# Kernel tuning notes

Measured on AMD Instinct MI355X. Metric: run time of the kernel, lower is better.

Reference implementation:

```python
import jax, jax.numpy as jnp
import numpy as np
from jax import lax

EPS = 1e-10

def _safe_norm(x):
    # torch remove_zeros: replace exact-zero norms with 1e-10
    n = jnp.linalg.norm(x, axis=-1, keepdims=True)
    return jnp.where(n != 0, n, jnp.full_like(n, EPS))

def setup_inputs() -> dict:
    key = jax.random.key(0)
    ks = jax.random.split(key, 5)
    S, B, D = 2048, 32, 512  # seq, batch, 2*hidden
    K = 147  # odd(max_entries/14)
    return {
        "encoder_outputs": jax.random.normal(ks[0], (S, B, D), dtype=jnp.float32),
        "state": jax.random.normal(ks[1], (B, D), dtype=jnp.float32),
        "previous_attention": jax.random.uniform(ks[2], (B, S), dtype=jnp.float32),
        "W_att": jax.random.normal(ks[3], (D, D), dtype=jnp.float32) / np.sqrt(D),
        "b_att": jax.random.normal(ks[4], (D,), dtype=jnp.float32) * 0.01,
        "conv_w": jnp.ones((1, 1, K), dtype=jnp.float32),
        "conv_b": jnp.zeros((1,), dtype=jnp.float32),
    }

def reference(encoder_outputs, state, previous_attention, W_att, b_att, conv_w, conv_b):
    S, B, D = encoder_outputs.shape
    # attended state via linear layer, then cosine-similarity weights (vectorized over seq)
    attended = state @ W_att.T + b_att                       # [B, D]
    ns = attended / _safe_norm(attended)                     # [B, D]
    ne = encoder_outputs / _safe_norm(encoder_outputs)       # [S, B, D]
    weights = jnp.einsum('bd,sbd->bs', ns, ne)               # [B, S]
    # conv1d time smoothing of previous attention (same-length, odd kernel)
    k = conv_w.shape[-1]
    pad = k // 2
    y = lax.conv_general_dilated(previous_attention[:, None, :], conv_w,
                                 window_strides=(1,), padding=[(pad, pad)])
    adjusted = jax.nn.relu(y[:, 0, :] + conv_b)              # [B, S]
    prev_probs = adjusted / jnp.sum(adjusted, axis=1, keepdims=True)
    adj = prev_probs * jax.nn.softmax(weights, axis=1)
    norm_w = adj / jnp.sum(adj, axis=1, keepdims=True)       # [B, S]
    applied = jnp.einsum('bs,sbd->bd', norm_w, encoder_outputs)  # [B, D]
    return applied, norm_w
```

## Files before the change

kernel.cpp:

```cpp
#include <hip/hip_runtime.h>
#include <hip/hip_bf16.h>
#include <math.h>


__device__ __forceinline__ float wave_sum(float v) {
    for (int off = 32; off; off >>= 1) v += __shfl_xor(v, off);
    return v;
}

__global__ __launch_bounds__(256) void front_kernel(
    const float* __restrict__ state, const float* __restrict__ W,
    const float* __restrict__ bias, const float* __restrict__ prev,
    const float* __restrict__ cw, const float* __restrict__ cb,
    float* __restrict__ attended, float* __restrict__ adj,
    int S, int D, int K) {
    __shared__ __align__(16) float smem[1024];
    int b = blockIdx.y;
    int t = threadIdx.x;

    if (blockIdx.x < 2) {
        if (t < D / 4)
            ((float4*)smem)[t] = ((const float4*)(state + (size_t)b * D))[t];
        __syncthreads();
        int d = blockIdx.x * 256 + t;
        const float4* Wrow = (const float4*)(W + (size_t)d * D);
        const float4* sv = (const float4*)smem;
        float acc = bias[d];
#pragma unroll 8
        for (int k = 0; k < 128; ++k) {
            float4 w4 = Wrow[k];
            float4 s4 = sv[k];
            acc += w4.x * s4.x + w4.y * s4.y + w4.z * s4.z + w4.w * s4.w;
        }
        attended[(size_t)b * D + d] = acc;
    } else {
        int s0 = (blockIdx.x - 2) * 256;
        int pad = K / 2;
        int seglen = 256 + K - 1;
        float* seg = smem;
        float* wk = smem + 512;
        for (int i = t; i < seglen; i += 256) {
            int s = s0 - pad + i;
            seg[i] = (s >= 0 && s < S) ? prev[(size_t)b * S + s] : 0.f;
        }
        for (int j = t; j < K; j += 256) wk[j] = cw[j];
        __syncthreads();
        float y = cb[0];
        for (int j = 0; j < K; ++j) y += seg[t + j] * wk[j];
        adj[(size_t)b * S + s0 + t] = fmaxf(y, 0.f);
    }
}

__global__ __launch_bounds__(256) void main_kernel(
    const float* __restrict__ e, const float* __restrict__ attended,
    const float* __restrict__ adj, float* __restrict__ partial,
    float* __restrict__ zbuf, float* __restrict__ u,
    int S, int B, int D, int CH) {
    int wave = threadIdx.x >> 6;
    int lane = threadIdx.x & 63;
    int c = blockIdx.x * 4 + wave;
    int b = blockIdx.y;

    const float4* att4 = (const float4*)(attended + (size_t)b * D);
    float4 a0 = att4[lane];
    float4 a1 = att4[lane + 64];
    float asq = a0.x * a0.x + a0.y * a0.y + a0.z * a0.z + a0.w * a0.w
              + a1.x * a1.x + a1.y * a1.y + a1.z * a1.z + a1.w * a1.w;
    asq = wave_sum(asq);
    float an = sqrtf(asq);
    if (an == 0.f) an = 1e-10f;
    float ainv = 1.f / an;
    float4 ns0, ns1;
    ns0.x = a0.x * ainv; ns0.y = a0.y * ainv; ns0.z = a0.z * ainv; ns0.w = a0.w * ainv;
    ns1.x = a1.x * ainv; ns1.y = a1.y * ainv; ns1.z = a1.z * ainv; ns1.w = a1.w * ainv;

    float4 acc0 = {0.f, 0.f, 0.f, 0.f};
    float4 acc1 = {0.f, 0.f, 0.f, 0.f};
    float z = 0.f;

    int s0 = c * CH;
    const float4* row4 = (const float4*)(e + ((size_t)s0 * B + b) * D);
    size_t rstride = (size_t)B * D / 4;

    float4 x0 = row4[lane];
    float4 x1 = row4[lane + 64];
    for (int i = 0; i < CH; ++i) {
        float4 nx0, nx1;
        if (i + 1 < CH) {
            nx0 = row4[rstride + lane];
            nx1 = row4[rstride + lane + 64];
        }
        float dot = x0.x * ns0.x + x0.y * ns0.y + x0.z * ns0.z + x0.w * ns0.w
                  + x1.x * ns1.x + x1.y * ns1.y + x1.z * ns1.z + x1.w * ns1.w;
        float sq  = x0.x * x0.x + x0.y * x0.y + x0.z * x0.z + x0.w * x0.w
                  + x1.x * x1.x + x1.y * x1.y + x1.z * x1.z + x1.w * x1.w;
        dot = wave_sum(dot);
        sq  = wave_sum(sq);
        float n = sqrtf(sq);
        if (n == 0.f) n = 1e-10f;
        float w = dot / n;
        float coef = adj[(size_t)b * S + s0 + i] * __expf(w);
        if (lane == 0) u[(size_t)b * S + s0 + i] = coef;
        acc0.x += coef * x0.x; acc0.y += coef * x0.y;
        acc0.z += coef * x0.z; acc0.w += coef * x0.w;
        acc1.x += coef * x1.x; acc1.y += coef * x1.y;
        acc1.z += coef * x1.z; acc1.w += coef * x1.w;
        z += coef;
        x0 = nx0; x1 = nx1;
        row4 += rstride;
    }

    float4* p4 = (float4*)(partial + ((size_t)c * B + b) * D);
    p4[lane] = acc0;
    p4[lane + 64] = acc1;
    if (lane == 0) zbuf[(size_t)c * B + b] = z;
}

__global__ __launch_bounds__(256) void combine_kernel(
    const float* __restrict__ partial, const float* __restrict__ zbuf,
    const float* __restrict__ u, float* __restrict__ applied,
    float* __restrict__ norm_w, int S, int B, int D, int NCB) {
    int b = blockIdx.x;
    int t = threadIdx.x;
    int lane = t & 63, wv = t >> 6;
    __shared__ float red[4];
    __shared__ float zsh;

    float zt = (t < NCB) ? zbuf[(size_t)t * B + b] : 0.f;
    zt = wave_sum(zt);
    if (lane == 0) red[wv] = zt;
    __syncthreads();
    if (t == 0) zsh = 1.f / (red[0] + red[1] + red[2] + red[3]);
    __syncthreads();
    float inv = zsh;

    if (t < D / 4) {
        float4 acc = {0.f, 0.f, 0.f, 0.f};
        const float4* p4 = (const float4*)partial;
        for (int c = 0; c < NCB; ++c) {
            float4 x = p4[((size_t)c * B + b) * (D / 4) + t];
            acc.x += x.x; acc.y += x.y; acc.z += x.z; acc.w += x.w;
        }
        acc.x *= inv; acc.y *= inv; acc.z *= inv; acc.w *= inv;
        ((float4*)(applied + (size_t)b * D))[t] = acc;
    }

    for (int s = t; s < S; s += 256)
        norm_w[(size_t)b * S + s] = u[(size_t)b * S + s] * inv;
}

extern "C" void kernel_launch(void* const* d_in, const int* in_sizes, int n_in,
                              void* d_out, int out_size, void* d_ws, size_t ws_size,
                              hipStream_t stream) {
    const float* enc   = (const float*)d_in[0];
    const float* state = (const float*)d_in[1];
    const float* prev  = (const float*)d_in[2];
    const float* W     = (const float*)d_in[3];
    const float* bias  = (const float*)d_in[4];
    const float* cw    = (const float*)d_in[5];
    const float* cb    = (const float*)d_in[6];

    const int S = in_sizes[0] / in_sizes[1];
    const int B = in_sizes[2] / S;
    const int D = in_sizes[1] / B;
    const int K = in_sizes[5];

    float* out     = (float*)d_out;
    float* applied = out;
    float* norm_w  = out + (size_t)B * D;

    const int NCB = 128;
    const int CH = S / NCB;

    float* ws       = (float*)d_ws;
    float* attended = ws;
    float* adj      = attended + (size_t)B * D;
    float* u        = adj + (size_t)B * S;
    float* zbuf     = u + (size_t)B * S;
    float* partial  = zbuf + (size_t)NCB * B;

    front_kernel<<<dim3(2 + S / 256, B), 256, 0, stream>>>(
        state, W, bias, prev, cw, cb, attended, adj, S, D, K);
    main_kernel<<<dim3(NCB / 4, B), 256, 0, stream>>>(
        enc, attended, adj, partial, zbuf, u, S, B, D, CH);
    combine_kernel<<<B, 256, 0, stream>>>(
        partial, zbuf, u, applied, norm_w, S, B, D, NCB);
}
```

Baseline: 252.3 us.

## Process four sequence rows per wave with 16-lane groups and precompute normalized state

New measurement: 265.3 us. 5.2% more time.

```diff
diff --git a/kernel.cpp b/kernel.cpp
--- a/kernel.cpp
+++ b/kernel.cpp
@@ -3,47 +3,61 @@
 #include <math.h>
 
 
+__device__ __forceinline__ float group16_sum(float v) {
+    v += __shfl_xor(v, 1);
+    v += __shfl_xor(v, 2);
+    v += __shfl_xor(v, 4);
+    v += __shfl_xor(v, 8);
+    return v;
+}
 __device__ __forceinline__ float wave_sum(float v) {
     for (int off = 32; off; off >>= 1) v += __shfl_xor(v, off);
     return v;
 }
 
-__global__ __launch_bounds__(256) void front_kernel(
+__global__ __launch_bounds__(512) void front_kernel(
     const float* __restrict__ state, const float* __restrict__ W,
     const float* __restrict__ bias, const float* __restrict__ prev,
     const float* __restrict__ cw, const float* __restrict__ cb,
-    float* __restrict__ attended, float* __restrict__ adj,
+    float* __restrict__ ns, float* __restrict__ adj,
     int S, int D, int K) {
-    __shared__ __align__(16) float smem[1024];
+    __shared__ __align__(16) float smem[824];
     int b = blockIdx.y;
     int t = threadIdx.x;
 
-    if (blockIdx.x < 2) {
+    if (blockIdx.x == 0) {
         if (t < D / 4)
             ((float4*)smem)[t] = ((const float4*)(state + (size_t)b * D))[t];
         __syncthreads();
-        int d = blockIdx.x * 256 + t;
-        const float4* Wrow = (const float4*)(W + (size_t)d * D);
+        const float4* Wrow = (const float4*)(W + (size_t)t * D);
         const float4* sv = (const float4*)smem;
-        float acc = bias[d];
+        float acc = bias[t];
 #pragma unroll 8
         for (int k = 0; k < 128; ++k) {
             float4 w4 = Wrow[k];
             float4 s4 = sv[k];
             acc += w4.x * s4.x + w4.y * s4.y + w4.z * s4.z + w4.w * s4.w;
         }
-        attended[(size_t)b * D + d] = acc;
+        float sq = wave_sum(acc * acc);
+        __shared__ float red[8];
+        int lane = t & 63, wv = t >> 6;
+        if (lane == 0) red[wv] = sq;
+        __syncthreads();
+        float total = red[0] + red[1] + red[2] + red[3]
+                    + red[4] + red[5] + red[6] + red[7];
+        float inv = (total == 0.f) ? 0.f : rsqrtf(total);
+        ns[(size_t)b * D + t] = acc * inv;
     } else {
-        int s0 = (blockIdx.x - 2) * 256;
+        int s0 = (blockIdx.x - 1) * 512;
         int pad = K / 2;
-        int seglen = 256 + K - 1;
+        int seglen = 512 + K - 1;
         float* seg = smem;
-        float* wk = smem + 512;
-        for (int i = t; i < seglen; i += 256) {
+        float* wk = smem + 664;
+        for (int i = t; i < seglen; i += 512) {
             int s = s0 - pad + i;
             seg[i] = (s >= 0 && s < S) ? prev[(size_t)b * S + s] : 0.f;
         }
-        for (int j = t; j < K; j += 256) wk[j] = cw[j];
+        for (int j = t; j < K; j += 512) wk[j] = cw[j];
         __syncthreads();
         float y = cb[0];
         for (int j = 0; j < K; ++j) y += seg[t + j] * wk[j];
@@ -52,68 +66,80 @@
 }
 
 __global__ __launch_bounds__(256) void main_kernel(
-    const float* __restrict__ e, const float* __restrict__ attended,
+    const float* __restrict__ e, const float* __restrict__ ns,
     const float* __restrict__ adj, float* __restrict__ partial,
     float* __restrict__ zbuf, float* __restrict__ u,
     int S, int B, int D, int CH) {
     int wave = threadIdx.x >> 6;
     int lane = threadIdx.x & 63;
-    int c = blockIdx.x * 4 + wave;
+    int r = lane >> 4;
+    int c = lane & 15;
+    int chunk = blockIdx.x * 4 + wave;
     int b = blockIdx.y;
-
-    const float4* att4 = (const float4*)(attended + (size_t)b * D);
-    float4 a0 = att4[lane];
-    float4 a1 = att4[lane + 64];
-    float asq = a0.x * a0.x + a0.y * a0.y + a0.z * a0.z + a0.w * a0.w
-              + a1.x * a1.x + a1.y * a1.y + a1.z * a1.z + a1.w * a1.w;
-    asq = wave_sum(asq);
-    float an = sqrtf(asq);
-    if (an == 0.f) an = 1e-10f;
-    float ainv = 1.f / an;
-    float4 ns0, ns1;
-    ns0.x = a0.x * ainv; ns0.y = a0.y * ainv; ns0.z = a0.z * ainv; ns0.w = a0.w * ainv;
-    ns1.x = a1.x * ainv; ns1.y = a1.y * ainv; ns1.z = a1.z * ainv; ns1.w = a1.w * ainv;
-
-    float4 acc0 = {0.f, 0.f, 0.f, 0.f};
-    float4 acc1 = {0.f, 0.f, 0.f, 0.f};
+    int s0 = chunk * CH;
+
+    const float4* ns4 = (const float4*)(ns + (size_t)b * D);
+    float4 nsv[8];
+#pragma unroll
+    for (int j = 0; j < 8; ++j) nsv[j] = ns4[c + 16 * j];
+
+    float4 acc[8];
+#pragma unroll
+    for (int j = 0; j < 8; ++j) acc[j] = make_float4(0.f, 0.f, 0.f, 0.f);
     float z = 0.f;
 
-    int s0 = c * CH;
-    const float4* row4 = (const float4*)(e + ((size_t)s0 * B + b) * D);
-    size_t rstride = (size_t)B * D / 4;
-
-    float4 x0 = row4[lane];
-    float4 x1 = row4[lane + 64];
-    for (int i = 0; i < CH; ++i) {
-        float4 nx0, nx1;
-        if (i + 1 < CH) {
-            nx0 = row4[rstride + lane];
-            nx1 = row4[rstride + lane + 64];
-        }
-        float dot = x0.x * ns0.x + x0.y * ns0.y + x0.z * ns0.z + x0.w * ns0.w
-                  + x1.x * ns1.x + x1.y * ns1.y + x1.z * ns1.z + x1.w * ns1.w;
-        float sq  = x0.x * x0.x + x0.y * x0.y + x0.z * x0.z + x0.w * x0.w
-                  + x1.x * x1.x + x1.y * x1.y + x1.z * x1.z + x1.w * x1.w;
-        dot = wave_sum(dot);
-        sq  = wave_sum(sq);
-        float n = sqrtf(sq);
-        if (n == 0.f) n = 1e-10f;
-        float w = dot / n;
-        float coef = adj[(size_t)b * S + s0 + i] * __expf(w);
-        if (lane == 0) u[(size_t)b * S + s0 + i] = coef;
-        acc0.x += coef * x0.x; acc0.y += coef * x0.y;
-        acc0.z += coef * x0.z; acc0.w += coef * x0.w;
-        acc1.x += coef * x1.x; acc1.y += coef * x1.y;
-        acc1.z += coef * x1.z; acc1.w += coef * x1.w;
+    size_t rowstride = (size_t)B * D / 4;
+    const float4* base = (const float4*)(e + ((size_t)(s0 + r) * B + b) * D);
+    const float* arow = adj + (size_t)b * S + s0;
+    float* urow = u + (size_t)b * S + s0;
+
+    for (int g = 0; g < 4; ++g) {
+        const float4* rp = base + (size_t)(4 * g) * rowstride;
+        float4 x[8];
+#pragma unroll
+        for (int j = 0; j < 8; ++j) x[j] = rp[c + 16 * j];
+        float dot = 0.f, sq = 0.f;
+#pragma unroll
+        for (int j = 0; j < 8; ++j) {
+            dot += x[j].x * nsv[j].x + x[j].y * nsv[j].y
+                 + x[j].z * nsv[j].z + x[j].w * nsv[j].w;
+            sq  += x[j].x * x[j].x + x[j].y * x[j].y
+                 + x[j].z * x[j].z + x[j].w * x[j].w;
+        }
+        dot = group16_sum(dot);
+        sq  = group16_sum(sq);
+        float winv = (sq == 0.f) ? 0.f : rsqrtf(sq);
+        float w = dot * winv;
+        float coef = arow[4 * g + r] * __expf(w);
+        if (c == 0) urow[4 * g + r] = coef;
         z += coef;
-        x0 = nx0; x1 = nx1;
-        row4 += rstride;
-    }
-
-    float4* p4 = (float4*)(partial + ((size_t)c * B + b) * D);
-    p4[lane] = acc0;
-    p4[lane + 64] = acc1;
-    if (lane == 0) zbuf[(size_t)c * B + b] = z;
+#pragma unroll
+        for (int j = 0; j < 8; ++j) {
+            acc[j].x += coef * x[j].x; acc[j].y += coef * x[j].y;
+            acc[j].z += coef * x[j].z; acc[j].w += coef * x[j].w;
+        }
+    }
+
+#pragma unroll
+    for (int j = 0; j < 8; ++j) {
+        acc[j].x += __shfl_xor(acc[j].x, 16);
+        acc[j].y += __shfl_xor(acc[j].y, 16);
+        acc[j].z += __shfl_xor(acc[j].z, 16);
+        acc[j].w += __shfl_xor(acc[j].w, 16);
+        acc[j].x += __shfl_xor(acc[j].x, 32);
+        acc[j].y += __shfl_xor(acc[j].y, 32);
+        acc[j].z += __shfl_xor(acc[j].z, 32);
+        acc[j].w += __shfl_xor(acc[j].w, 32);
+    }
+    z += __shfl_xor(z, 16);
+    z += __shfl_xor(z, 32);
+
+    float4* p4 = (float4*)(partial + ((size_t)chunk * B + b) * D);
+    if (r == 0) {
+#pragma unroll
+        for (int j = 0; j < 8; ++j) p4[c + 16 * j] = acc[j];
+    }
+    if (lane == 0) zbuf[(size_t)chunk * B + b] = z;
 }
 
 __global__ __launch_bounds__(256) void combine_kernel(
@@ -137,8 +163,8 @@
     if (t < D / 4) {
         float4 acc = {0.f, 0.f, 0.f, 0.f};
         const float4* p4 = (const float4*)partial;
-        for (int c = 0; c < NCB; ++c) {
-            float4 x = p4[((size_t)c * B + b) * (D / 4) + t];
+        for (int cix = 0; cix < NCB; ++cix) {
+            float4 x = p4[((size_t)cix * B + b) * (D / 4) + t];
             acc.x += x.x; acc.y += x.y; acc.z += x.z; acc.w += x.w;
         }
         acc.x *= inv; acc.y *= inv; acc.z *= inv; acc.w *= inv;
@@ -172,17 +198,17 @@
     const int NCB = 128;
     const int CH = S / NCB;
 
-    float* ws       = (float*)d_ws;
-    float* attended = ws;
-    float* adj      = attended + (size_t)B * D;
-    float* u        = adj + (size_t)B * S;
-    float* zbuf     = u + (size_t)B * S;
-    float* partial  = zbuf + (size_t)NCB * B;
-
-    front_kernel<<<dim3(2 + S / 256, B), 256, 0, stream>>>(
-        state, W, bias, prev, cw, cb, attended, adj, S, D, K);
+    float* ws      = (float*)d_ws;
+    float* ns      = ws;
+    float* adj     = ns + (size_t)B * D;
+    float* u       = adj + (size_t)B * S;
+    float* zbuf    = u + (size_t)B * S;
+    float* partial = zbuf + (size_t)NCB * B;
+
+    front_kernel<<<dim3(1 + S / 512, B), 512, 0, stream>>>(
+        state, W, bias, prev, cw, cb, ns, adj, S, D, K);
     main_kernel<<<dim3(NCB / 4, B), 256, 0, stream>>>(
-        enc, attended, adj, partial, zbuf, u, S, B, D, CH);
+        enc, ns, adj, partial, zbuf, u, S, B, D, CH);
     combine_kernel<<<B, 256, 0, stream>>>(
         partial, zbuf, u, applied, norm_w, S, B, D, NCB);
 }
```
